# Kernel tuning notes

Hardware: AMD Instinct MI355X
Metric: run time of the kernel (lower is better)

The kernel has to match this reference:

```python
import jax, jax.numpy as jnp
import numpy as np

H, C = 3, 64
HC = H * C
D_IN = 256
N_A, N_T, N_U = 10000, 100000, 50000
E0, E1, E2 = 200000, 300000, 300000
B = 32
OUT = 2
NEG_SLOPE = 0.2


def setup_inputs() -> dict:
    key = jax.random.key(0)
    ks = jax.random.split(key, 24)

    def p(k, shape, fan_in):
        return jax.random.normal(k, shape, jnp.float32) * (1.0 / np.sqrt(fan_in))

    inp = {}
    inp["x_article"] = jax.random.normal(ks[0], (N_A, D_IN), jnp.float32)
    inp["x_tweet"] = jax.random.normal(ks[1], (N_T, D_IN), jnp.float32)
    inp["x_user"] = jax.random.normal(ks[2], (N_U, D_IN), jnp.float32)
    # layer-1 GATConv params, stacked over the 3 edge types
    inp["Wsrc1"] = p(ks[3], (3, D_IN, HC), D_IN)
    inp["Wdst1"] = p(ks[4], (3, D_IN, HC), D_IN)
    inp["as1"] = p(ks[5], (3, H, C), C)
    inp["ad1"] = p(ks[6], (3, H, C), C)
    inp["b1"] = jnp.zeros((3, HC), jnp.float32)
    # layer-2 GATConv params (inputs are H*C wide after layer 1)
    inp["Wsrc2"] = p(ks[7], (3, HC, HC), HC)
    inp["Wdst2"] = p(ks[8], (3, HC, HC), HC)
    inp["as2"] = p(ks[9], (3, H, C), C)
    inp["ad2"] = p(ks[10], (3, H, C), C)
    inp["b2"] = jnp.zeros((3, HC), jnp.float32)
    inp["linW"] = p(ks[11], (HC * 3, OUT), HC * 3)
    inp["linb"] = jnp.zeros((OUT,), jnp.float32)
    # edge lists: (tweet->article), (user->tweet), (tweet->user)
    inp["src0"] = jax.random.randint(ks[12], (E0,), 0, N_T, jnp.int32)
    inp["dst0"] = jax.random.randint(ks[13], (E0,), 0, N_A, jnp.int32)
    inp["src1"] = jax.random.randint(ks[14], (E1,), 0, N_U, jnp.int32)
    inp["dst1"] = jax.random.randint(ks[15], (E1,), 0, N_T, jnp.int32)
    inp["src2"] = jax.random.randint(ks[16], (E2,), 0, N_T, jnp.int32)
    inp["dst2"] = jax.random.randint(ks[17], (E2,), 0, N_U, jnp.int32)
    inp["batch_article"] = jnp.sort(jax.random.randint(ks[18], (N_A,), 0, B, jnp.int32))
    inp["batch_tweet"] = jnp.sort(jax.random.randint(ks[19], (N_T,), 0, B, jnp.int32))
    inp["batch_user"] = jnp.sort(jax.random.randint(ks[20], (N_U,), 0, B, jnp.int32))
    inp["num_graphs"] = B
    return inp


def _gat(xs, xd, src, dst, Ws, Wd, a_s, a_d, b):
    """Bipartite PyG GATConv, concat heads, add_self_loops=False."""
    nd = xd.shape[0]
    hs = (xs @ Ws).reshape(xs.shape[0], H, C)   # [Ns,H,C]
    hd = (xd @ Wd).reshape(xd.shape[0], H, C)   # [Nd,H,C]
    als = jnp.sum(hs * a_s[None], axis=-1)      # [Ns,H]
    ald = jnp.sum(hd * a_d[None], axis=-1)      # [Nd,H]
    e = jax.nn.leaky_relu(als[src] + ald[dst], negative_slope=NEG_SLOPE)  # [E,H]
    m = jax.lax.stop_gradient(jax.ops.segment_max(e, dst, num_segments=nd))
    m = jnp.where(jnp.isfinite(m), m, 0.0)      # guard empty segments
    ex = jnp.exp(e - m[dst])
    den = jax.ops.segment_sum(ex, dst, num_segments=nd)
    alpha = ex / den[dst]                       # segment softmax over in-edges
    msg = (hs[src] * alpha[:, :, None]).reshape(src.shape[0], HC)
    return jax.ops.segment_sum(msg, dst, num_segments=nd) + b


def _hetero_layer(xa, xt, xu, src0, dst0, src1, dst1, src2, dst2, Ws, Wd, a_s, a_d, b):
    oa = _gat(xt, xa, src0, dst0, Ws[0], Wd[0], a_s[0], a_d[0], b[0])  # tweet->article
    ot = _gat(xu, xt, src1, dst1, Ws[1], Wd[1], a_s[1], a_d[1], b[1])  # user->tweet
    ou = _gat(xt, xu, src2, dst2, Ws[2], Wd[2], a_s[2], a_d[2], b[2])  # tweet->user
    return jax.nn.relu(oa), jax.nn.relu(ot), jax.nn.relu(ou)


def _mean_pool(x, batch, num_graphs):
    s = jax.ops.segment_sum(x, batch, num_segments=num_graphs)
    cnt = jax.ops.segment_sum(jnp.ones((x.shape[0],), x.dtype), batch, num_segments=num_graphs)
    return s / jnp.maximum(cnt, 1.0)[:, None]


def reference(x_article, x_tweet, x_user, Wsrc1, Wdst1, as1, ad1, b1,
              Wsrc2, Wdst2, as2, ad2, b2, linW, linb,
              src0, dst0, src1, dst1, src2, dst2,
              batch_article, batch_tweet, batch_user, num_graphs):
    xa, xt, xu = _hetero_layer(x_article, x_tweet, x_user,
                               src0, dst0, src1, dst1, src2, dst2,
                               Wsrc1, Wdst1, as1, ad1, b1)
    xa, xt, xu = _hetero_layer(xa, xt, xu,
                               src0, dst0, src1, dst1, src2, dst2,
                               Wsrc2, Wdst2, as2, ad2, b2)
    pa = _mean_pool(xa, batch_article, num_graphs)
    pt = _mean_pool(xt, batch_tweet, num_graphs)
    pu = _mean_pool(xu, batch_user, num_graphs)
    x = jnp.concatenate([pa, pt, pu], axis=1)  # [B, 3*H*C]
    # dropout p=0.5 is identity in eval mode
    return x @ linW + linb
```

## Files before the change

### kernel.cpp

```cpp
#include <hip/hip_runtime.h>
#include <cstdint>

#define H 3
#define C 64
#define HC 192
#define NEG 0.2f

#define N_A 10000
#define N_T 100000
#define N_U 50000
#define E0c 200000
#define E1c 300000
#define E2c 300000

#define BM 128
#define BN 64
#define BK 16

__global__ __launch_bounds__(256) void gemm_f32(
    const float* __restrict__ A, const float* __restrict__ W,
    float* __restrict__ Cmat, int N, int K) {
  __shared__ float As[BK][BM + 4];
  __shared__ float Bs[BK][BN + 4];
  const int tid = threadIdx.x;
  const int bm = blockIdx.x * BM;
  const int bn = blockIdx.y * BN;
  const int tx = tid & 15, ty = tid >> 4;
  float acc[8][4];
#pragma unroll
  for (int i = 0; i < 8; ++i)
#pragma unroll
    for (int j = 0; j < 4; ++j) acc[i][j] = 0.f;

  for (int k0 = 0; k0 < K; k0 += BK) {
#pragma unroll
    for (int i = 0; i < 2; ++i) {
      int idx = tid + i * 256;
      int m = idx >> 2, k4 = idx & 3;
      int gm = bm + m;
      float4 v = make_float4(0.f, 0.f, 0.f, 0.f);
      if (gm < N) v = *(const float4*)(A + (size_t)gm * K + k0 + k4 * 4);
      As[k4 * 4 + 0][m] = v.x;
      As[k4 * 4 + 1][m] = v.y;
      As[k4 * 4 + 2][m] = v.z;
      As[k4 * 4 + 3][m] = v.w;
    }
    {
      int k = tid >> 4, n4 = tid & 15;
      float4 v = *(const float4*)(W + (size_t)(k0 + k) * HC + bn + n4 * 4);
      *(float4*)&Bs[k][n4 * 4] = v;
    }
    __syncthreads();
#pragma unroll
    for (int k = 0; k < BK; ++k) {
      float4 a0 = *(const float4*)&As[k][ty * 8];
      float4 a1 = *(const float4*)&As[k][ty * 8 + 4];
      float4 b = *(const float4*)&Bs[k][tx * 4];
      float av[8] = {a0.x, a0.y, a0.z, a0.w, a1.x, a1.y, a1.z, a1.w};
      float bv[4] = {b.x, b.y, b.z, b.w};
#pragma unroll
      for (int i = 0; i < 8; ++i)
#pragma unroll
        for (int j = 0; j < 4; ++j) acc[i][j] += av[i] * bv[j];
    }
    __syncthreads();
  }
#pragma unroll
  for (int i = 0; i < 8; ++i) {
    int gm = bm + ty * 8 + i;
    if (gm < N) {
      float4 v = make_float4(acc[i][0], acc[i][1], acc[i][2], acc[i][3]);
      *(float4*)(Cmat + (size_t)gm * HC + bn + tx * 4) = v;
    }
  }
}

__global__ void wvec_kernel(const float* __restrict__ W,
                            const float* __restrict__ a,
                            float* __restrict__ wv, int K) {
  int k = blockIdx.x * blockDim.x + threadIdx.x;
  if (k >= K) return;
#pragma unroll
  for (int h = 0; h < H; ++h) {
    float s = 0.f;
    for (int c = 0; c < C; ++c) s += W[(size_t)k * HC + h * C + c] * a[h * C + c];
    wv[k * H + h] = s;
  }
}

__global__ void attn_proj(const float* __restrict__ x,
                          const float* __restrict__ wv,
                          float* __restrict__ out, int N, int K) {
  int lane = threadIdx.x & 63;
  int node = (blockIdx.x * blockDim.x + threadIdx.x) >> 6;
  if (node >= N) return;
  float p0 = 0.f, p1 = 0.f, p2 = 0.f;
  for (int k = lane; k < K; k += 64) {
    float xv = x[(size_t)node * K + k];
    p0 += xv * wv[k * 3 + 0];
    p1 += xv * wv[k * 3 + 1];
    p2 += xv * wv[k * 3 + 2];
  }
#pragma unroll
  for (int off = 32; off; off >>= 1) {
    p0 += __shfl_xor(p0, off);
    p1 += __shfl_xor(p1, off);
    p2 += __shfl_xor(p2, off);
  }
  if (lane == 0) {
    out[node * 3 + 0] = p0;
    out[node * 3 + 1] = p1;
    out[node * 3 + 2] = p2;
  }
}

__global__ void csr_count(const int* __restrict__ dst, int* __restrict__ pos, int E) {
  int e = blockIdx.x * blockDim.x + threadIdx.x;
  if (e < E) atomicAdd(&pos[dst[e]], 1);
}

__global__ void scan_block_sums(const int* __restrict__ deg, int* __restrict__ bsum, int n) {
  __shared__ int sdata[256];
  int base = blockIdx.x * 1024;
  int t = threadIdx.x;
  int s = 0;
  for (int i = t; i < 1024; i += 256) {
    int idx = base + i;
    s += (idx < n) ? deg[idx] : 0;
  }
  sdata[t] = s;
  __syncthreads();
  for (int o = 128; o; o >>= 1) {
    if (t < o) sdata[t] += sdata[t + o];
    __syncthreads();
  }
  if (t == 0) bsum[blockIdx.x] = sdata[0];
}

__global__ void scan_bsum(int* __restrict__ bsum, int nb) {
  __shared__ int sh[1024];
  int t = threadIdx.x;
  int v = (t < nb) ? bsum[t] : 0;
  sh[t] = v;
  __syncthreads();
  for (int o = 1; o < 1024; o <<= 1) {
    int x = (t >= o) ? sh[t - o] : 0;
    __syncthreads();
    sh[t] += x;
    __syncthreads();
  }
  if (t < nb) bsum[t] = sh[t] - v;
}

__global__ void scan_chunks(const int* __restrict__ deg, const int* __restrict__ bsum,
                            int* __restrict__ rowptr, int* __restrict__ pos, int n) {
  __shared__ int sh[1024];
  int t = threadIdx.x;
  int idx = blockIdx.x * 1024 + t;
  int v = (idx < n) ? deg[idx] : 0;
  sh[t] = v;
  __syncthreads();
  for (int o = 1; o < 1024; o <<= 1) {
    int x = (t >= o) ? sh[t - o] : 0;
    __syncthreads();
    sh[t] += x;
    __syncthreads();
  }
  if (idx < n) {
    int ex = sh[t] - v + bsum[blockIdx.x];
    rowptr[idx] = ex;
    pos[idx] = ex;
  }
  if (idx == n - 1) rowptr[n] = sh[t] + bsum[blockIdx.x];
}

__global__ void csr_fill(const int* __restrict__ src, const int* __restrict__ dst,
                         int* __restrict__ pos, int* __restrict__ csrc, int E) {
  int e = blockIdx.x * blockDim.x + threadIdx.x;
  if (e >= E) return;
  int slot = atomicAdd(&pos[dst[e]], 1);
  csrc[slot] = src[e];
}

__global__ __launch_bounds__(256) void gat_gather(
    const int* __restrict__ rowptr, const int* __restrict__ csrc,
    const float* __restrict__ als, const float* __restrict__ ald,
    const float* __restrict__ hs, const float* __restrict__ bias,
    float* __restrict__ outx, int Nd) {
  int lane = threadIdx.x & 63;
  int d = (blockIdx.x * 256 + threadIdx.x) >> 6;
  if (d >= Nd) return;
  int beg = rowptr[d], end = rowptr[d + 1];
  float ad0 = ald[d * 3 + 0], ad1 = ald[d * 3 + 1], ad2 = ald[d * 3 + 2];

  float m0 = -1e30f, m1 = -1e30f, m2 = -1e30f;
  for (int j = beg + lane; j < end; j += 64) {
    int s = csrc[j];
    float l0 = als[s * 3 + 0] + ad0; l0 = l0 > 0.f ? l0 : NEG * l0;
    float l1 = als[s * 3 + 1] + ad1; l1 = l1 > 0.f ? l1 : NEG * l1;
    float l2 = als[s * 3 + 2] + ad2; l2 = l2 > 0.f ? l2 : NEG * l2;
    m0 = fmaxf(m0, l0); m1 = fmaxf(m1, l1); m2 = fmaxf(m2, l2);
  }
#pragma unroll
  for (int o = 32; o; o >>= 1) {
    m0 = fmaxf(m0, __shfl_xor(m0, o));
    m1 = fmaxf(m1, __shfl_xor(m1, o));
    m2 = fmaxf(m2, __shfl_xor(m2, o));
  }

  float den0 = 0.f, den1 = 0.f, den2 = 0.f;
  float acc0 = 0.f, acc1 = 0.f, acc2 = 0.f;
  for (int j = beg; j < end; ++j) {
    int s = csrc[j];
    float l0 = als[s * 3 + 0] + ad0; l0 = l0 > 0.f ? l0 : NEG * l0;
    float l1 = als[s * 3 + 1] + ad1; l1 = l1 > 0.f ? l1 : NEG * l1;
    float l2 = als[s * 3 + 2] + ad2; l2 = l2 > 0.f ? l2 : NEG * l2;
    float w0 = __expf(l0 - m0);
    float w1 = __expf(l1 - m1);
    float w2 = __expf(l2 - m2);
    den0 += w0; den1 += w1; den2 += w2;
    const float* hr = hs + (size_t)s * HC;
    acc0 += w0 * hr[lane];
    acc1 += w1 * hr[64 + lane];
    acc2 += w2 * hr[128 + lane];
  }
  float i0 = den0 > 0.f ? 1.f / den0 : 0.f;
  float i1 = den1 > 0.f ? 1.f / den1 : 0.f;
  float i2 = den2 > 0.f ? 1.f / den2 : 0.f;
  float* orow = outx + (size_t)d * HC;
  orow[lane]       = fmaxf(acc0 * i0 + bias[lane], 0.f);
  orow[64 + lane]  = fmaxf(acc1 * i1 + bias[64 + lane], 0.f);
  orow[128 + lane] = fmaxf(acc2 * i2 + bias[128 + lane], 0.f);
}

__global__ void pool_kernel(const float* __restrict__ x, const int* __restrict__ batch,
                            float* __restrict__ pool, float* __restrict__ cnt, int N) {
  int c = threadIdx.x;
  int n0 = blockIdx.x * 64;
  int nend = min(n0 + 64, N);
  float acc = 0.f, cacc = 0.f;
  int cur = batch[n0];
  for (int n = n0; n < nend; ++n) {
    int bg = batch[n];
    if (bg != cur) {
      atomicAdd(&pool[(size_t)cur * HC + c], acc);
      if (c == 0) atomicAdd(&cnt[cur], cacc);
      acc = 0.f;
      cacc = 0.f;
      cur = bg;
    }
    acc += x[(size_t)n * HC + c];
    cacc += 1.f;
  }
  atomicAdd(&pool[(size_t)cur * HC + c], acc);
  if (c == 0) atomicAdd(&cnt[cur], cacc);
}

__global__ void final_linear(const float* __restrict__ pool, const float* __restrict__ cnt,
                             const float* __restrict__ linW, const float* __restrict__ linb,
                             float* __restrict__ out) {
  int tid = threadIdx.x;
  if (tid >= 64) return;
  int b = tid >> 1, o = tid & 1;
  float s = linb[o];
#pragma unroll
  for (int t = 0; t < 3; ++t) {
    float inv = 1.f / fmaxf(cnt[t * 32 + b], 1.f);
    const float* p = pool + ((size_t)t * 32 + b) * HC;
    for (int j = 0; j < HC; ++j)
      s += p[j] * inv * linW[(t * HC + j) * 2 + o];
  }
  out[b * 2 + o] = s;
}

extern "C" void kernel_launch(void* const* d_in, const int* in_sizes, int n_in,
                              void* d_out, int out_size, void* d_ws, size_t ws_size,
                              hipStream_t stream) {
  const float* xA = (const float*)d_in[0];
  const float* xT = (const float*)d_in[1];
  const float* xU = (const float*)d_in[2];
  const float* Ws1 = (const float*)d_in[3];
  const float* Wd1 = (const float*)d_in[4];
  const float* as1 = (const float*)d_in[5];
  const float* ad1 = (const float*)d_in[6];
  const float* b1 = (const float*)d_in[7];
  const float* Ws2 = (const float*)d_in[8];
  const float* Wd2 = (const float*)d_in[9];
  const float* as2 = (const float*)d_in[10];
  const float* ad2 = (const float*)d_in[11];
  const float* b2 = (const float*)d_in[12];
  const float* linW = (const float*)d_in[13];
  const float* linb = (const float*)d_in[14];
  const int* srcs[3] = {(const int*)d_in[15], (const int*)d_in[17], (const int*)d_in[19]};
  const int* dsts[3] = {(const int*)d_in[16], (const int*)d_in[18], (const int*)d_in[20]};
  const int* batA = (const int*)d_in[21];
  const int* batT = (const int*)d_in[22];
  const int* batU = (const int*)d_in[23];

  float* ws = (float*)d_ws;
  size_t off = 0;
  auto alloc = [&](size_t n) { float* p = ws + off; off += n; return p; };
  float* hs = alloc((size_t)N_T * HC);
  float* als = alloc((size_t)N_T * H);
  float* ald = alloc((size_t)N_T * H);
  float* x1a = alloc((size_t)N_A * HC);
  float* x1t = alloc((size_t)N_T * HC);
  float* x1u = alloc((size_t)N_U * HC);
  float* x2a = alloc((size_t)N_A * HC);
  float* x2t = alloc((size_t)N_T * HC);
  float* x2u = alloc((size_t)N_U * HC);
  float* wsv = alloc(256 * 3);
  float* wdv = alloc(256 * 3);
  float* pool = alloc(3 * 32 * HC);
  float* cnt = alloc(96);
  int* rowptr[3];
  int* pos[3];
  int* csrc[3];
  const int Ecnt[3] = {E0c, E1c, E2c};
  const int NdA[3] = {N_A, N_T, N_U};
  const int NsA[3] = {N_T, N_U, N_T};
  for (int t = 0; t < 3; ++t) {
    rowptr[t] = (int*)alloc(NdA[t] + 1);
    pos[t] = (int*)alloc(NdA[t]);
    csrc[t] = (int*)alloc(Ecnt[t]);
  }
  int* bsum = (int*)alloc(1024);
  (void)ws_size; (void)in_sizes; (void)n_in; (void)out_size;

  for (int t = 0; t < 3; ++t) {
    int Nd = NdA[t], E = Ecnt[t];
    int nb = (Nd + 1023) / 1024;
    hipMemsetAsync(pos[t], 0, (size_t)Nd * sizeof(int), stream);
    csr_count<<<(E + 255) / 256, 256, 0, stream>>>(dsts[t], pos[t], E);
    scan_block_sums<<<nb, 256, 0, stream>>>(pos[t], bsum, Nd);
    scan_bsum<<<1, 1024, 0, stream>>>(bsum, nb);
    scan_chunks<<<nb, 1024, 0, stream>>>(pos[t], bsum, rowptr[t], pos[t], Nd);
    csr_fill<<<(E + 255) / 256, 256, 0, stream>>>(srcs[t], dsts[t], pos[t], csrc[t], E);
  }

  for (int layer = 0; layer < 2; ++layer) {
    int K = layer ? HC : 256;
    const float* Wsl = layer ? Ws2 : Ws1;
    const float* Wdl = layer ? Wd2 : Wd1;
    const float* asl = layer ? as2 : as1;
    const float* adl = layer ? ad2 : ad1;
    const float* bl = layer ? b2 : b1;
    const float* xsrc[3];
    const float* xdst[3];
    float* outx[3];
    if (layer == 0) {
      xsrc[0] = xT; xsrc[1] = xU; xsrc[2] = xT;
      xdst[0] = xA; xdst[1] = xT; xdst[2] = xU;
      outx[0] = x1a; outx[1] = x1t; outx[2] = x1u;
    } else {
      xsrc[0] = x1t; xsrc[1] = x1u; xsrc[2] = x1t;
      xdst[0] = x1a; xdst[1] = x1t; xdst[2] = x1u;
      outx[0] = x2a; outx[1] = x2t; outx[2] = x2u;
    }
    for (int t = 0; t < 3; ++t) {
      int Ns = NsA[t], Nd = NdA[t];
      const float* Wt = Wsl + (size_t)t * K * HC;
      const float* Wdt = Wdl + (size_t)t * K * HC;
      wvec_kernel<<<1, 256, 0, stream>>>(Wt, asl + t * HC, wsv, K);
      wvec_kernel<<<1, 256, 0, stream>>>(Wdt, adl + t * HC, wdv, K);
      gemm_f32<<<dim3((Ns + BM - 1) / BM, HC / BN), 256, 0, stream>>>(xsrc[t], Wt, hs, Ns, K);
      attn_proj<<<(Ns + 3) / 4, 256, 0, stream>>>(xsrc[t], wsv, als, Ns, K);
      attn_proj<<<(Nd + 3) / 4, 256, 0, stream>>>(xdst[t], wdv, ald, Nd, K);
      gat_gather<<<(Nd + 3) / 4, 256, 0, stream>>>(rowptr[t], csrc[t], als, ald, hs,
                                                   bl + t * HC, outx[t], Nd);
    }
  }

  hipMemsetAsync(pool, 0, 3 * 32 * HC * sizeof(float), stream);
  hipMemsetAsync(cnt, 0, 96 * sizeof(float), stream);
  pool_kernel<<<(N_A + 63) / 64, 192, 0, stream>>>(x2a, batA, pool + 0, cnt + 0, N_A);
  pool_kernel<<<(N_T + 63) / 64, 192, 0, stream>>>(x2t, batT, pool + 32 * HC, cnt + 32, N_T);
  pool_kernel<<<(N_U + 63) / 64, 192, 0, stream>>>(x2u, batU, pool + 64 * HC, cnt + 64, N_U);
  final_linear<<<1, 64, 0, stream>>>(pool, cnt, linW, linb, (float*)d_out);
}
```

Before: 1.724 ms.

## Replace FP32 SIMT GEMM with split-bf16x3 MFMA GEMM over full 192-column tile

The source-feature projection GEMM moves from a scalar FP32 register-tiled kernel to MFMA bf16 instructions. Each FP32 value is split into high and low bf16 parts, and three MFMAs per tile approximate FP32 accuracy. A small kernel transposes W beforehand so both operands are K-contiguous in shared memory, and each block now covers all 192 output columns. The split conversion and the extra transpose launch cost ALU work and a little memory traffic. Accuracy is slightly below true FP32 because the low-by-low term is dropped.

```diff
diff --git a/kernel.cpp b/kernel.cpp
--- a/kernel.cpp
+++ b/kernel.cpp
@@ -13,64 +13,117 @@
 #define E1c 300000
 #define E2c 300000
 
-#define BM 128
-#define BN 64
-#define BK 16
-
-__global__ __launch_bounds__(256) void gemm_f32(
-    const float* __restrict__ A, const float* __restrict__ W,
-    float* __restrict__ Cmat, int N, int K) {
-  __shared__ float As[BK][BM + 4];
-  __shared__ float Bs[BK][BN + 4];
+typedef __attribute__((ext_vector_type(8))) short short8;
+typedef __attribute__((ext_vector_type(4))) float f32x4;
+
+__device__ __forceinline__ void split1(float f, ushort& h, ushort& l) {
+  unsigned u = __float_as_uint(f);
+  unsigned r = u + 0x7FFFu + ((u >> 16) & 1u);
+  h = (ushort)(r >> 16);
+  float fhi = __uint_as_float((unsigned)h << 16);
+  float d = f - fhi;
+  unsigned u2 = __float_as_uint(d);
+  unsigned r2 = u2 + 0x7FFFu + ((u2 >> 16) & 1u);
+  l = (ushort)(r2 >> 16);
+}
+__device__ __forceinline__ void split4(float4 v, ushort4& h, ushort4& l) {
+  split1(v.x, h.x, l.x);
+  split1(v.y, h.y, l.y);
+  split1(v.z, h.z, l.z);
+  split1(v.w, h.w, l.w);
+}
+
+__global__ void wtrans_kernel(const float* __restrict__ W, float* __restrict__ Wt, int K) {
+  int i = blockIdx.x * blockDim.x + threadIdx.x;
+  if (i >= K * HC) return;
+  int c = i / K, k = i - c * K;
+  Wt[i] = W[(size_t)k * HC + c];
+}
+
+#define GBM 128
+#define GBK 32
+#define PAD 40
+
+__global__ __launch_bounds__(256) void gemm_bf16x3(
+    const float* __restrict__ A, const float* __restrict__ Wt,
+    float* __restrict__ Cmat, int M, int K) {
+  __shared__ __align__(16) ushort AsH[GBM][PAD];
+  __shared__ __align__(16) ushort AsL[GBM][PAD];
+  __shared__ __align__(16) ushort WsH[HC][PAD];
+  __shared__ __align__(16) ushort WsL[HC][PAD];
   const int tid = threadIdx.x;
-  const int bm = blockIdx.x * BM;
-  const int bn = blockIdx.y * BN;
-  const int tx = tid & 15, ty = tid >> 4;
-  float acc[8][4];
-#pragma unroll
-  for (int i = 0; i < 8; ++i)
-#pragma unroll
-    for (int j = 0; j < 4; ++j) acc[i][j] = 0.f;
-
-  for (int k0 = 0; k0 < K; k0 += BK) {
-#pragma unroll
-    for (int i = 0; i < 2; ++i) {
-      int idx = tid + i * 256;
-      int m = idx >> 2, k4 = idx & 3;
-      int gm = bm + m;
+  const int lane = tid & 63;
+  const int wid = tid >> 6;
+  const int wr = wid >> 1;
+  const int wc = wid & 1;
+  const int bm = blockIdx.x * GBM;
+  const int l15 = lane & 15;
+  const int kgrp = lane >> 4;
+
+  f32x4 acc[4][6];
+#pragma unroll
+  for (int i = 0; i < 4; ++i)
+#pragma unroll
+    for (int j = 0; j < 6; ++j) acc[i][j] = (f32x4){0.f, 0.f, 0.f, 0.f};
+
+  for (int k0 = 0; k0 < K; k0 += GBK) {
+#pragma unroll
+    for (int i = 0; i < 4; ++i) {
+      int fi = tid + i * 256;
+      int row = fi >> 3, kq = fi & 7;
+      int gm = bm + row;
       float4 v = make_float4(0.f, 0.f, 0.f, 0.f);
-      if (gm < N) v = *(const float4*)(A + (size_t)gm * K + k0 + k4 * 4);
-      As[k4 * 4 + 0][m] = v.x;
-      As[k4 * 4 + 1][m] = v.y;
-      As[k4 * 4 + 2][m] = v.z;
-      As[k4 * 4 + 3][m] = v.w;
-    }
-    {
-      int k = tid >> 4, n4 = tid & 15;
-      float4 v = *(const float4*)(W + (size_t)(k0 + k) * HC + bn + n4 * 4);
-      *(float4*)&Bs[k][n4 * 4] = v;
-    }
-    __syncthreads();
-#pragma unroll
-    for (int k = 0; k < BK; ++k) {
-      float4 a0 = *(const float4*)&As[k][ty * 8];
-      float4 a1 = *(const float4*)&As[k][ty * 8 + 4];
-      float4 b = *(const float4*)&Bs[k][tx * 4];
-      float av[8] = {a0.x, a0.y, a0.z, a0.w, a1.x, a1.y, a1.z, a1.w};
-      float bv[4] = {b.x, b.y, b.z, b.w};
-#pragma unroll
-      for (int i = 0; i < 8; ++i)
-#pragma unroll
-        for (int j = 0; j < 4; ++j) acc[i][j] += av[i] * bv[j];
-    }
-    __syncthreads();
-  }
-#pragma unroll
-  for (int i = 0; i < 8; ++i) {
-    int gm = bm + ty * 8 + i;
-    if (gm < N) {
-      float4 v = make_float4(acc[i][0], acc[i][1], acc[i][2], acc[i][3]);
-      *(float4*)(Cmat + (size_t)gm * HC + bn + tx * 4) = v;
+      if (gm < M) v = *(const float4*)(A + (size_t)gm * K + k0 + kq * 4);
+      ushort4 h, l;
+      split4(v, h, l);
+      *(ushort4*)&AsH[row][kq * 4] = h;
+      *(ushort4*)&AsL[row][kq * 4] = l;
+    }
+#pragma unroll
+    for (int i = 0; i < 6; ++i) {
+      int fi = tid + i * 256;
+      int col = fi >> 3, kq = fi & 7;
+      float4 v = *(const float4*)(Wt + (size_t)col * K + k0 + kq * 4);
+      ushort4 h, l;
+      split4(v, h, l);
+      *(ushort4*)&WsH[col][kq * 4] = h;
+      *(ushort4*)&WsL[col][kq * 4] = l;
+    }
+    __syncthreads();
+
+    short8 aH[4], aL[4];
+#pragma unroll
+    for (int rf = 0; rf < 4; ++rf) {
+      int row = wr * 64 + rf * 16 + l15;
+      aH[rf] = *(const short8*)&AsH[row][kgrp * 8];
+      aL[rf] = *(const short8*)&AsL[row][kgrp * 8];
+    }
+#pragma unroll
+    for (int cf = 0; cf < 6; ++cf) {
+      int col = wc * 96 + cf * 16 + l15;
+      short8 bH = *(const short8*)&WsH[col][kgrp * 8];
+      short8 bL = *(const short8*)&WsL[col][kgrp * 8];
+#pragma unroll
+      for (int rf = 0; rf < 4; ++rf) {
+        acc[rf][cf] = __builtin_amdgcn_mfma_f32_16x16x32_bf16(aH[rf], bH, acc[rf][cf], 0, 0, 0);
+        acc[rf][cf] = __builtin_amdgcn_mfma_f32_16x16x32_bf16(aL[rf], bH, acc[rf][cf], 0, 0, 0);
+        acc[rf][cf] = __builtin_amdgcn_mfma_f32_16x16x32_bf16(aH[rf], bL, acc[rf][cf], 0, 0, 0);
+      }
+    }
+    __syncthreads();
+  }
+
+#pragma unroll
+  for (int rf = 0; rf < 4; ++rf) {
+#pragma unroll
+    for (int r = 0; r < 4; ++r) {
+      int row = bm + wr * 64 + rf * 16 + kgrp * 4 + r;
+      if (row < M) {
+#pragma unroll
+        for (int cf = 0; cf < 6; ++cf) {
+          Cmat[(size_t)row * HC + wc * 96 + cf * 16 + l15] = acc[rf][cf][r];
+        }
+      }
     }
   }
 }
@@ -313,6 +366,7 @@
   float* wdv = alloc(256 * 3);
   float* pool = alloc(3 * 32 * HC);
   float* cnt = alloc(96);
+  float* wt = alloc((size_t)HC * 256);
   int* rowptr[3];
   int* pos[3];
   int* csrc[3];
@@ -363,7 +417,8 @@
       const float* Wdt = Wdl + (size_t)t * K * HC;
       wvec_kernel<<<1, 256, 0, stream>>>(Wt, asl + t * HC, wsv, K);
       wvec_kernel<<<1, 256, 0, stream>>>(Wdt, adl + t * HC, wdv, K);
-      gemm_f32<<<dim3((Ns + BM - 1) / BM, HC / BN), 256, 0, stream>>>(xsrc[t], Wt, hs, Ns, K);
+      wtrans_kernel<<<(K * HC + 255) / 256, 256, 0, stream>>>(Wt, wt, K);
+      gemm_bf16x3<<<(Ns + GBM - 1) / GBM, 256, 0, stream>>>(xsrc[t], wt, hs, Ns, K);
       attn_proj<<<(Ns + 3) / 4, 256, 0, stream>>>(xsrc[t], wsv, als, Ns, K);
       attn_proj<<<(Nd + 3) / 4, 256, 0, stream>>>(xdst[t], wdv, ald, Nd, K);
       gat_gather<<<(Nd + 3) / 4, 256, 0, stream>>>(rowptr[t], csrc[t], als, ald, hs,
```

Result: faster. 1.516 ms (-12.1%).
